# Performance work log

Measured on AMD Instinct MI355X. Metric: run time of the kernel, lower is better.

The kernel has to match this reference:

```python
import jax, jax.numpy as jnp
import numpy as np

EPS = 1e-5

def _bn(x, g, b):
    m = x.mean(axis=0)
    v = x.var(axis=0)  # biased, matches torch BN training normalization
    return g * (x - m) * jax.lax.rsqrt(v + EPS) + b

def _mlp(x, W1, b1, g1, be1, W2, b2, g2, be2):
    h = jax.nn.relu(_bn(x @ W1 + b1, g1, be1))
    return jax.nn.relu(_bn(h @ W2 + b2, g2, be2))

def setup_inputs() -> dict:
    key = jax.random.key(0)
    ks = jax.random.split(key, 12)
    n, e, d, de = 100000, 1600000, 128, 16
    def lin(k, fan_in, fan_out):
        bound = 1.0 / np.sqrt(fan_in)
        k1, k2 = jax.random.split(k)
        W = jax.random.uniform(k1, (fan_in, fan_out), jnp.float32, -bound, bound)
        b = jax.random.uniform(k2, (fan_out,), jnp.float32, -bound, bound)
        return W, b
    msg_W1, msg_b1 = lin(ks[0], 2 * d + de, d)
    msg_W2, msg_b2 = lin(ks[1], d, d)
    upd_W1, upd_b1 = lin(ks[2], 3 * d, d)
    upd_W2, upd_b2 = lin(ks[3], d, d)
    return {
        "h": jax.random.normal(ks[4], (n, d), jnp.float32),
        "edge_index": jax.random.randint(ks[5], (2, e), 0, n, jnp.int64),
        "edge_attr": jax.random.normal(ks[6], (e, de), jnp.float32),
        "msg_W1": msg_W1, "msg_b1": msg_b1,
        "msg_g1": jnp.ones((d,)), "msg_be1": jnp.zeros((d,)),
        "msg_W2": msg_W2, "msg_b2": msg_b2,
        "msg_g2": jnp.ones((d,)), "msg_be2": jnp.zeros((d,)),
        "upd_W1": upd_W1, "upd_b1": upd_b1,
        "upd_g1": jnp.ones((d,)), "upd_be1": jnp.zeros((d,)),
        "upd_W2": upd_W2, "upd_b2": upd_b2,
        "upd_g2": jnp.ones((d,)), "upd_be2": jnp.zeros((d,)),
    }

def reference(h, edge_index, edge_attr,
              msg_W1, msg_b1, msg_g1, msg_be1, msg_W2, msg_b2, msg_g2, msg_be2,
              upd_W1, upd_b1, upd_g1, upd_be1, upd_W2, upd_b2, upd_g2, upd_be2):
    alpha = 0.5
    n = h.shape[0]
    src = edge_index[0]
    dst = edge_index[1]
    h_i = h[src]  # (e, d)
    h_j = h[dst]  # (e, d)
    msg_args = (msg_W1, msg_b1, msg_g1, msg_be1, msg_W2, msg_b2, msg_g2, msg_be2)
    m_st = _mlp(jnp.concatenate([h_i, h_j, edge_attr], axis=-1), *msg_args)
    m_ts = _mlp(jnp.concatenate([h_j, h_i, edge_attr], axis=-1), *msg_args)
    # NOTE: original code scatters both directions by source nodes (faithful)
    a_st = jax.ops.segment_sum(m_st, src, num_segments=n)
    a_ts = jax.ops.segment_sum(m_ts, src, num_segments=n)
    upd_in = jnp.concatenate([h, alpha * a_st, (1.0 - alpha) * a_ts], axis=-1)
    return _mlp(upd_in, upd_W1, upd_b1, upd_g1, upd_be1, upd_W2, upd_b2, upd_g2, upd_be2)
```

## Files before the change

kernel.cpp:

```cpp
#include <hip/hip_runtime.h>

#define EPS_BN 1e-5f

typedef __bf16 bf16x8 __attribute__((ext_vector_type(8)));
typedef float f32x4 __attribute__((ext_vector_type(4)));
typedef unsigned short us8 __attribute__((ext_vector_type(8)));
typedef unsigned int u32x4 __attribute__((ext_vector_type(4)));

__device__ __forceinline__ unsigned short f2bf(float x) {
  unsigned u = __builtin_bit_cast(unsigned, x);
  unsigned r = (u + 0x7fffu + ((u >> 16) & 1u)) >> 16;
  return (unsigned short)r;
}
__device__ __forceinline__ unsigned pack2bf(float a, float b) {
  return (unsigned)f2bf(a) | ((unsigned)f2bf(b) << 16);
}
__device__ __forceinline__ unsigned long long pack4bf(float a, float b, float c, float d) {
  return (unsigned long long)pack2bf(a, b) | ((unsigned long long)pack2bf(c, d) << 32);
}
__device__ __forceinline__ float ubf(unsigned short u) {
  return __builtin_bit_cast(float, (unsigned)u << 16);
}

template <bool ABF16>
__global__ __launch_bounds__(256) void node_mfma(
    const void* A0, const void* A1, const void* A2,
    const float* __restrict__ W, float s0, float s1, float s2,
    float* __restrict__ C, int n, int dostats,
    float* __restrict__ sum_out, float* __restrict__ ssq_out, int nk) {
  __shared__ unsigned short WT[128][136];
  int tid = threadIdx.x;
  int lid = tid & 63, w = tid >> 6, lr = lid & 15, lq = lid >> 4;
  long rbase = (long)blockIdx.x * 64 + 16 * w;

  const void* As[3] = {A0, A1, A2};
  float ss[3] = {s0, s1, s2};
  f32x4 acc[8];
  #pragma unroll
  for (int nf = 0; nf < 8; ++nf) acc[nf] = f32x4{0.f, 0.f, 0.f, 0.f};

  long r = rbase + lr;
  bool rv = (r < n);
  long rl = rv ? r : 0;

  for (int c = 0; c < nk; ++c) {
    if (c) __syncthreads();
    const float* Wc = W + (long)c * 16384;
    float sc = ss[c];
    for (int i = tid; i < 16384; i += 256) {
      int k = i >> 7, cc = i & 127;
      WT[cc][k] = f2bf(Wc[i] * sc);
    }
    __syncthreads();

    bf16x8 af[4];
    if (ABF16) {
      const us8* Ar = (const us8*)((const unsigned short*)As[c] + rl * 128);
      #pragma unroll
      for (int ks = 0; ks < 4; ++ks) {
        us8 v = Ar[ks * 4 + lq];
        if (!rv) v = us8{0, 0, 0, 0, 0, 0, 0, 0};
        af[ks] = __builtin_bit_cast(bf16x8, v);
      }
    } else {
      const float* Ar = (const float*)As[c] + rl * 128;
      #pragma unroll
      for (int ks = 0; ks < 4; ++ks) {
        int e0 = 32 * ks + 8 * lq;
        float4 x = *(const float4*)(Ar + e0);
        float4 y = *(const float4*)(Ar + e0 + 4);
        u32x4 t;
        t[0] = pack2bf(x.x, x.y); t[1] = pack2bf(x.z, x.w);
        t[2] = pack2bf(y.x, y.y); t[3] = pack2bf(y.z, y.w);
        if (!rv) { t[0] = 0; t[1] = 0; t[2] = 0; t[3] = 0; }
        af[ks] = __builtin_bit_cast(bf16x8, t);
      }
    }
    #pragma unroll
    for (int nf = 0; nf < 8; ++nf) {
      const char* bp = (const char*)&WT[16 * nf + lr][0];
      #pragma unroll
      for (int ks = 0; ks < 4; ++ks) {
        bf16x8 bf = *(const bf16x8*)(bp + ks * 64 + lq * 16);
        acc[nf] = __builtin_amdgcn_mfma_f32_16x16x32_bf16(af[ks], bf, acc[nf], 0, 0, 0);
      }
    }
  }

  float lsum[8], lssq[8];
  #pragma unroll
  for (int nf = 0; nf < 8; ++nf) { lsum[nf] = 0.f; lssq[nf] = 0.f; }
  #pragma unroll
  for (int nf = 0; nf < 8; ++nf) {
    #pragma unroll
    for (int i = 0; i < 4; ++i) {
      long nd = rbase + 4 * lq + i;
      if (nd < n) {
        float v = acc[nf][i];
        C[nd * 128 + 16 * nf + lr] = v;
        lsum[nf] += v; lssq[nf] += v * v;
      }
    }
  }
  if (dostats) {
    #pragma unroll
    for (int nf = 0; nf < 8; ++nf) {
      float v0 = lsum[nf]; v0 += __shfl_xor(v0, 16); v0 += __shfl_xor(v0, 32);
      float v1 = lssq[nf]; v1 += __shfl_xor(v1, 16); v1 += __shfl_xor(v1, 32);
      if (lq == 0) {
        atomicAdd(&sum_out[16 * nf + lr], v0);
        atomicAdd(&ssq_out[16 * nf + lr], v1);
      }
    }
  }
}

__global__ __launch_bounds__(256) void msg_stats1(
    const float* __restrict__ P, const float* __restrict__ Q,
    const float* __restrict__ EA, const float* __restrict__ W1e,
    const int* __restrict__ SRC, const int* __restrict__ DST, long E,
    float* __restrict__ stats) {
  __shared__ float Wel[16][128];
  __shared__ float red[32][16];
  int tid = threadIdx.x;
  for (int i = tid; i < 16 * 128; i += 256) ((float*)Wel)[i] = W1e[i];
  for (int i = tid; i < 512; i += 256) ((float*)red)[i] = 0.f;
  __syncthreads();
  int c4 = tid & 31, grp = tid >> 5;
  const float4* P4 = (const float4*)P;
  const float4* Q4 = (const float4*)Q;
  float4 s_st = {0,0,0,0}, q_st = {0,0,0,0}, s_ts = {0,0,0,0}, q_ts = {0,0,0,0};
  long stride = (long)gridDim.x * 8;
  for (long e = (long)blockIdx.x * 8 + grp; e < E; e += stride) {
    int s = SRC[e], t = DST[e];
    float4 Ps = P4[(long)s * 32 + c4];
    float4 Qt = Q4[(long)t * 32 + c4];
    float4 Pt = P4[(long)t * 32 + c4];
    float4 Qs = Q4[(long)s * 32 + c4];
    float rx = 0.f, ry = 0.f, rz = 0.f, rw = 0.f;
    const float* eap = EA + e * 16;
    #pragma unroll
    for (int k = 0; k < 16; ++k) {
      float f = eap[k];
      const float4 w4 = *(const float4*)&Wel[k][c4 * 4];
      rx = fmaf(f, w4.x, rx); ry = fmaf(f, w4.y, ry);
      rz = fmaf(f, w4.z, rz); rw = fmaf(f, w4.w, rw);
    }
    float zx = Ps.x + Qt.x + rx, zy = Ps.y + Qt.y + ry, zz = Ps.z + Qt.z + rz, zw = Ps.w + Qt.w + rw;
    s_st.x += zx; s_st.y += zy; s_st.z += zz; s_st.w += zw;
    q_st.x += zx * zx; q_st.y += zy * zy; q_st.z += zz * zz; q_st.w += zw * zw;
    float ux = Pt.x + Qs.x + rx, uy = Pt.y + Qs.y + ry, uz = Pt.z + Qs.z + rz, uw = Pt.w + Qs.w + rw;
    s_ts.x += ux; s_ts.y += uy; s_ts.z += uz; s_ts.w += uw;
    q_ts.x += ux * ux; q_ts.y += uy * uy; q_ts.z += uz * uz; q_ts.w += uw * uw;
  }
  atomicAdd(&red[c4][0], s_st.x);  atomicAdd(&red[c4][1], s_st.y);
  atomicAdd(&red[c4][2], s_st.z);  atomicAdd(&red[c4][3], s_st.w);
  atomicAdd(&red[c4][4], q_st.x);  atomicAdd(&red[c4][5], q_st.y);
  atomicAdd(&red[c4][6], q_st.z);  atomicAdd(&red[c4][7], q_st.w);
  atomicAdd(&red[c4][8], s_ts.x);  atomicAdd(&red[c4][9], s_ts.y);
  atomicAdd(&red[c4][10], s_ts.z); atomicAdd(&red[c4][11], s_ts.w);
  atomicAdd(&red[c4][12], q_ts.x); atomicAdd(&red[c4][13], q_ts.y);
  atomicAdd(&red[c4][14], q_ts.z); atomicAdd(&red[c4][15], q_ts.w);
  __syncthreads();
  #pragma unroll
  for (int rep = 0; rep < 2; ++rep) {
    int j = rep * 256 + tid;
    int cc = j >> 4, k = j & 15, group = k >> 2, comp = k & 3;
    atomicAdd(&stats[group * 128 + cc * 4 + comp], red[cc][k]);
  }
}

__global__ __launch_bounds__(256) void prescale_pq(
    const float* __restrict__ X, const float* __restrict__ sca,
    const float* __restrict__ scb,
    unsigned* __restrict__ outA, unsigned* __restrict__ outB, long nrows) {
  long gid = (long)blockIdx.x * 256 + threadIdx.x;
  int c2 = (int)(gid & 63);
  float a0 = sca[2 * c2], a1 = sca[2 * c2 + 1];
  float b0 = scb[2 * c2], b1 = scb[2 * c2 + 1];
  const float2* X2 = (const float2*)X;
  long rstride = ((long)gridDim.x * 256) >> 6;
  for (long row = gid >> 6; row < nrows; row += rstride) {
    float2 x = X2[row * 64 + c2];
    outA[row * 64 + c2] = pack2bf(x.x * a0, x.y * a1);
    outB[row * 64 + c2] = pack2bf(x.x * b0, x.y * b1);
  }
}

__global__ __launch_bounds__(256) void prescale_relu(
    const float* __restrict__ X, const float* __restrict__ scsh,
    unsigned* __restrict__ out, long nrows) {
  long gid = (long)blockIdx.x * 256 + threadIdx.x;
  int c2 = (int)(gid & 63);
  float s0 = scsh[2 * c2], s1 = scsh[2 * c2 + 1];
  float h0 = scsh[128 + 2 * c2], h1 = scsh[128 + 2 * c2 + 1];
  const float2* X2 = (const float2*)X;
  long rstride = ((long)gridDim.x * 256) >> 6;
  for (long row = gid >> 6; row < nrows; row += rstride) {
    float2 x = X2[row * 64 + c2];
    out[row * 64 + c2] = pack2bf(fmaxf(fmaf(x.x, s0, h0), 0.f),
                                 fmaxf(fmaf(x.y, s1, h1), 0.f));
  }
}

__global__ __launch_bounds__(256) void rmat_scaled(
    const float* __restrict__ EA, const float* __restrict__ W1e,
    const float* __restrict__ sc1,
    unsigned* __restrict__ Rst, unsigned* __restrict__ Rts, long E) {
  long gid = (long)blockIdx.x * 256 + threadIdx.x;
  int c2 = (int)(gid & 63);
  int ch = 2 * c2;
  float wa[16], wb[16];
  #pragma unroll
  for (int k = 0; k < 16; ++k) { wa[k] = W1e[k * 128 + ch]; wb[k] = W1e[k * 128 + ch + 1]; }
  float sa_st = sc1[ch],       sb_st = sc1[ch + 1];
  float ha_st = sc1[128 + ch], hb_st = sc1[128 + ch + 1];
  float sa_ts = sc1[256 + ch], sb_ts = sc1[256 + ch + 1];
  float ha_ts = sc1[384 + ch], hb_ts = sc1[384 + ch + 1];
  long estride = ((long)gridDim.x * 256) >> 6;
  for (long e = gid >> 6; e < E; e += estride) {
    const float* eap = EA + e * 16;
    float ra = 0.f, rb = 0.f;
    #pragma unroll
    for (int k = 0; k < 16; ++k) { ra = fmaf(eap[k], wa[k], ra); rb = fmaf(eap[k], wb[k], rb); }
    Rst[e * 64 + c2] = pack2bf(fmaf(ra, sa_st, ha_st), fmaf(rb, sb_st, hb_st));
    Rts[e * 64 + c2] = pack2bf(fmaf(ra, sa_ts, ha_ts), fmaf(rb, sb_ts, hb_ts));
  }
}

template <bool SCATTER>
__global__ __launch_bounds__(256) void msg2(
    const unsigned short* __restrict__ Pst, const unsigned short* __restrict__ Qst,
    const unsigned short* __restrict__ Pts, const unsigned short* __restrict__ Qts,
    const unsigned short* __restrict__ Rst, const unsigned short* __restrict__ Rts,
    const float* __restrict__ W2,
    const int* __restrict__ SRC, const int* __restrict__ DST, long E,
    const float* __restrict__ sc2, float* __restrict__ stats2,
    float* __restrict__ a_st, float* __restrict__ a_ts) {
  __shared__ unsigned short W2T[128][136];
  int tid = threadIdx.x;
  for (int i = tid; i < 16384; i += 256) {
    int k = i >> 7, c = i & 127;
    W2T[c][k] = f2bf(W2[i]);
  }
  __syncthreads();
  int lid = tid & 63, w = tid >> 6, lr = lid & 15, lq = lid >> 4;

  float s2st[8], h2st[8], s2ts[8], h2ts[8];
  float sum_st[8], ssq_st[8], sum_ts[8], ssq_ts[8];
  if constexpr (SCATTER) {
    #pragma unroll
    for (int nf = 0; nf < 8; ++nf) {
      int ch = 16 * nf + lr;
      s2st[nf] = sc2[ch];       h2st[nf] = sc2[128 + ch];
      s2ts[nf] = sc2[256 + ch]; h2ts[nf] = sc2[384 + ch];
    }
  } else {
    #pragma unroll
    for (int nf = 0; nf < 8; ++nf) {
      sum_st[nf] = 0.f; ssq_st[nf] = 0.f; sum_ts[nf] = 0.f; ssq_ts[nf] = 0.f;
    }
  }

  for (long wbase = (long)blockIdx.x * 64 + 16 * w; wbase < E;
       wbase += (long)gridDim.x * 64) {
    long e = wbase + lr;
    bool ev = (e < E);
    long el = ev ? e : (E - 1);
    int s = SRC[el], t = DST[el];
    const us8* PstR = (const us8*)(Pst + (long)s * 128);
    const us8* QstR = (const us8*)(Qst + (long)t * 128);
    const us8* PtsR = (const us8*)(Pts + (long)t * 128);
    const us8* QtsR = (const us8*)(Qts + (long)s * 128);
    const us8* RstR = (const us8*)(Rst + el * 128);
    const us8* RtsR = (const us8*)(Rts + el * 128);

    bf16x8 afst[4], afts[4];
    #pragma unroll
    for (int ks = 0; ks < 4; ++ks) {
      int ci = ks * 4 + lq;
      us8 p1 = PstR[ci], q1 = QstR[ci], r1 = RstR[ci];
      us8 p2 = PtsR[ci], q2 = QtsR[ci], r2 = RtsR[ci];
      u32x4 t1, t2;
      #pragma unroll
      for (int jj = 0; jj < 4; ++jj) {
        float a0 = fmaxf(ubf(p1[2 * jj]) + ubf(q1[2 * jj]) + ubf(r1[2 * jj]), 0.f);
        float a1 = fmaxf(ubf(p1[2 * jj + 1]) + ubf(q1[2 * jj + 1]) + ubf(r1[2 * jj + 1]), 0.f);
        float b0 = fmaxf(ubf(p2[2 * jj]) + ubf(q2[2 * jj]) + ubf(r2[2 * jj]), 0.f);
        float b1 = fmaxf(ubf(p2[2 * jj + 1]) + ubf(q2[2 * jj + 1]) + ubf(r2[2 * jj + 1]), 0.f);
        t1[jj] = pack2bf(a0, a1);
        t2[jj] = pack2bf(b0, b1);
      }
      if (!ev) { t1[0]=0; t1[1]=0; t1[2]=0; t1[3]=0; t2[0]=0; t2[1]=0; t2[2]=0; t2[3]=0; }
      afst[ks] = __builtin_bit_cast(bf16x8, t1);
      afts[ks] = __builtin_bit_cast(bf16x8, t2);
    }

    int srow[4];
    if constexpr (SCATTER) {
      #pragma unroll
      for (int i = 0; i < 4; ++i) {
        long er = wbase + 4 * lq + i;
        srow[i] = (er < E) ? SRC[er] : -1;
      }
    }

    #pragma unroll
    for (int nf = 0; nf < 8; ++nf) {
      f32x4 acc_st = {0.f, 0.f, 0.f, 0.f};
      f32x4 acc_ts = {0.f, 0.f, 0.f, 0.f};
      const char* bp = (const char*)&W2T[16 * nf + lr][0];
      #pragma unroll
      for (int ks = 0; ks < 4; ++ks) {
        bf16x8 bf = *(const bf16x8*)(bp + ks * 64 + lq * 16);
        acc_st = __builtin_amdgcn_mfma_f32_16x16x32_bf16(afst[ks], bf, acc_st, 0, 0, 0);
        acc_ts = __builtin_amdgcn_mfma_f32_16x16x32_bf16(afts[ks], bf, acc_ts, 0, 0, 0);
      }
      if constexpr (SCATTER) {
        int ch = 16 * nf + lr;
        #pragma unroll
        for (int i = 0; i < 4; ++i) {
          if (srow[i] >= 0) {
            float m1 = fmaxf(fmaf(acc_st[i], s2st[nf], h2st[nf]), 0.f);
            float m2 = fmaxf(fmaf(acc_ts[i], s2ts[nf], h2ts[nf]), 0.f);
            if (m1 > 0.f) atomicAdd(&a_st[(long)srow[i] * 128 + ch], m1);
            if (m2 > 0.f) atomicAdd(&a_ts[(long)srow[i] * 128 + ch], m2);
          }
        }
      } else {
        #pragma unroll
        for (int i = 0; i < 4; ++i) {
          sum_st[nf] += acc_st[i]; ssq_st[nf] += acc_st[i] * acc_st[i];
          sum_ts[nf] += acc_ts[i]; ssq_ts[nf] += acc_ts[i] * acc_ts[i];
        }
      }
    }
  }

  if constexpr (!SCATTER) {
    #pragma unroll
    for (int nf = 0; nf < 8; ++nf) {
      float v0 = sum_st[nf]; v0 += __shfl_xor(v0, 16); v0 += __shfl_xor(v0, 32);
      float v1 = ssq_st[nf]; v1 += __shfl_xor(v1, 16); v1 += __shfl_xor(v1, 32);
      float v2 = sum_ts[nf]; v2 += __shfl_xor(v2, 16); v2 += __shfl_xor(v2, 32);
      float v3 = ssq_ts[nf]; v3 += __shfl_xor(v3, 16); v3 += __shfl_xor(v3, 32);
      if (lq == 0) {
        int ch = 16 * nf + lr;
        atomicAdd(&stats2[ch], v0);
        atomicAdd(&stats2[128 + ch], v1);
        atomicAdd(&stats2[256 + ch], v2);
        atomicAdd(&stats2[384 + ch], v3);
      }
    }
  }
}

template <bool SCATTER>
__global__ __launch_bounds__(256) void msg_mfma_kernel(
    const float* __restrict__ P, const float* __restrict__ Q,
    const float* __restrict__ EA, const float* __restrict__ W1e,
    const float* __restrict__ W2,
    const int* __restrict__ SRC, const int* __restrict__ DST, long E,
    const float* __restrict__ sc1, const float* __restrict__ sc2,
    float* __restrict__ stats2,
    float* __restrict__ a_st, float* __restrict__ a_ts) {
  __shared__ unsigned short W2T[128][136];
  __shared__ unsigned short Ast[64][136];
  __shared__ unsigned short Ats[64][136];
  __shared__ float Wel[16][128];
  __shared__ int sArr[64];

  int tid = threadIdx.x;
  int c4 = tid & 31;
  int slot = tid >> 5;
  int lid = tid & 63;
  int w = tid >> 6;
  int lr = lid & 15;
  int lq = lid >> 4;

  for (int i = tid; i < 16 * 128; i += 256) ((float*)Wel)[i] = W1e[i];
  #pragma unroll
  for (int i = 0; i < 64; ++i) {
    int idx = i * 256 + tid;
    int k = idx >> 7, n = idx & 127;
    W2T[n][k] = f2bf(W2[idx]);
  }

  const float4* sc1v = (const float4*)sc1;
  float4 scst = sc1v[c4], shst = sc1v[32 + c4];
  float4 scts = sc1v[64 + c4], shts = sc1v[96 + c4];

  float s2st[8], h2st[8], s2ts[8], h2ts[8];
  if constexpr (SCATTER) {
    #pragma unroll
    for (int nf = 0; nf < 8; ++nf) {
      int ch = 16 * nf + lr;
      s2st[nf] = sc2[ch];       h2st[nf] = sc2[128 + ch];
      s2ts[nf] = sc2[256 + ch]; h2ts[nf] = sc2[384 + ch];
    }
  }
  float ssum_st[8], sssq_st[8], ssum_ts[8], sssq_ts[8];
  if constexpr (!SCATTER) {
    #pragma unroll
    for (int nf = 0; nf < 8; ++nf) {
      ssum_st[nf] = 0.f; sssq_st[nf] = 0.f; ssum_ts[nf] = 0.f; sssq_ts[nf] = 0.f;
    }
  }

  const float4* P4 = (const float4*)P;
  const float4* Q4 = (const float4*)Q;

  for (long tb = (long)blockIdx.x * 64; tb < E; tb += (long)gridDim.x * 64) {
    int nE = (int)(E - tb < 64 ? E - tb : 64);
    __syncthreads();
    #pragma unroll 2
    for (int rep = 0; rep < 8; ++rep) {
      int er = rep * 8 + slot;
      if (er < nE) {
        long e = tb + er;
        int s = SRC[e], t = DST[e];
        if (SCATTER && c4 == 0) sArr[er] = s;
        float4 Ps = P4[(long)s * 32 + c4];
        float4 Qt = Q4[(long)t * 32 + c4];
        float4 Pt = P4[(long)t * 32 + c4];
        float4 Qs = Q4[(long)s * 32 + c4];
        float rx = 0.f, ry = 0.f, rz = 0.f, rw = 0.f;
        const float* eap = EA + e * 16;
        #pragma unroll
        for (int k = 0; k < 16; ++k) {
          float f = eap[k];
          const float4 w4 = *(const float4*)&Wel[k][c4 * 4];
          rx = fmaf(f, w4.x, rx); ry = fmaf(f, w4.y, ry);
          rz = fmaf(f, w4.z, rz); rw = fmaf(f, w4.w, rw);
        }
        float ax = fmaxf(fmaf(Ps.x + Qt.x + rx, scst.x, shst.x), 0.f);
        float ay = fmaxf(fmaf(Ps.y + Qt.y + ry, scst.y, shst.y), 0.f);
        float az = fmaxf(fmaf(Ps.z + Qt.z + rz, scst.z, shst.z), 0.f);
        float aw = fmaxf(fmaf(Ps.w + Qt.w + rw, scst.w, shst.w), 0.f);
        *(unsigned long long*)&Ast[er][c4 * 4] = pack4bf(ax, ay, az, aw);
        float bx = fmaxf(fmaf(Pt.x + Qs.x + rx, scts.x, shts.x), 0.f);
        float by = fmaxf(fmaf(Pt.y + Qs.y + ry, scts.y, shts.y), 0.f);
        float bz = fmaxf(fmaf(Pt.z + Qs.z + rz, scts.z, shts.z), 0.f);
        float bw = fmaxf(fmaf(Pt.w + Qs.w + rw, scts.w, shts.w), 0.f);
        *(unsigned long long*)&Ats[er][c4 * 4] = pack4bf(bx, by, bz, bw);
      } else {
        *(unsigned long long*)&Ast[er][c4 * 4] = 0ull;
        *(unsigned long long*)&Ats[er][c4 * 4] = 0ull;
      }
    }
    __syncthreads();

    int arow = 16 * w + lr;
    const char* astp = (const char*)&Ast[arow][0];
    const char* atsp = (const char*)&Ats[arow][0];
    int acolb = lq * 16;
    bf16x8 afst[4], afts[4];
    #pragma unroll
    for (int ks = 0; ks < 4; ++ks) {
      afst[ks] = *(const bf16x8*)(astp + ks * 64 + acolb);
      afts[ks] = *(const bf16x8*)(atsp + ks * 64 + acolb);
    }
    int srow[4];
    if constexpr (SCATTER) {
      #pragma unroll
      for (int i = 0; i < 4; ++i) {
        int row = 16 * w + 4 * lq + i;
        srow[i] = (row < nE) ? sArr[row] : -1;
      }
    }
    #pragma unroll
    for (int nf = 0; nf < 8; ++nf) {
      f32x4 acc_st = {0.f, 0.f, 0.f, 0.f};
      f32x4 acc_ts = {0.f, 0.f, 0.f, 0.f};
      const char* bp = (const char*)&W2T[16 * nf + lr][0];
      #pragma unroll
      for (int ks = 0; ks < 4; ++ks) {
        bf16x8 bf = *(const bf16x8*)(bp + ks * 64 + acolb);
        acc_st = __builtin_amdgcn_mfma_f32_16x16x32_bf16(afst[ks], bf, acc_st, 0, 0, 0);
        acc_ts = __builtin_amdgcn_mfma_f32_16x16x32_bf16(afts[ks], bf, acc_ts, 0, 0, 0);
      }
      if constexpr (SCATTER) {
        int ch = 16 * nf + lr;
        #pragma unroll
        for (int i = 0; i < 4; ++i) {
          if (srow[i] >= 0) {
            float m1 = fmaxf(fmaf(acc_st[i], s2st[nf], h2st[nf]), 0.f);
            float m2 = fmaxf(fmaf(acc_ts[i], s2ts[nf], h2ts[nf]), 0.f);
            if (m1 > 0.f) atomicAdd(&a_st[(long)srow[i] * 128 + ch], m1);
            if (m2 > 0.f) atomicAdd(&a_ts[(long)srow[i] * 128 + ch], m2);
          }
        }
      } else {
        #pragma unroll
        for (int i = 0; i < 4; ++i) {
          ssum_st[nf] += acc_st[i]; sssq_st[nf] += acc_st[i] * acc_st[i];
          ssum_ts[nf] += acc_ts[i]; sssq_ts[nf] += acc_ts[i] * acc_ts[i];
        }
      }
    }
  }

  if constexpr (!SCATTER) {
    #pragma unroll
    for (int nf = 0; nf < 8; ++nf) {
      float v0 = ssum_st[nf]; v0 += __shfl_xor(v0, 16); v0 += __shfl_xor(v0, 32);
      float v1 = sssq_st[nf]; v1 += __shfl_xor(v1, 16); v1 += __shfl_xor(v1, 32);
      float v2 = ssum_ts[nf]; v2 += __shfl_xor(v2, 16); v2 += __shfl_xor(v2, 32);
      float v3 = sssq_ts[nf]; v3 += __shfl_xor(v3, 16); v3 += __shfl_xor(v3, 32);
      if (lq == 0) {
        int ch = 16 * nf + lr;
        atomicAdd(&stats2[ch], v0);
        atomicAdd(&stats2[128 + ch], v1);
        atomicAdd(&stats2[256 + ch], v2);
        atomicAdd(&stats2[384 + ch], v3);
      }
    }
  }
}

__global__ void bn_finalize(const float* __restrict__ sum, const float* __restrict__ ssq,
                            float invN, const float* __restrict__ g,
                            const float* __restrict__ be,
                            float* __restrict__ sc, float* __restrict__ sh) {
  int j = threadIdx.x;
  float m = sum[j] * invN;
  float v = ssq[j] * invN - m * m;
  float s = g[j] * rsqrtf(v + EPS_BN);
  sc[j] = s;
  sh[j] = be[j] - m * s;
}

__global__ __launch_bounds__(256) void bn_relu_out(
    const float* __restrict__ U2, const float* __restrict__ scsh,
    float* __restrict__ out, long total) {
  long i = (long)blockIdx.x * blockDim.x + threadIdx.x;
  long stride = (long)gridDim.x * blockDim.x;
  for (; i < total; i += stride) {
    int j = (int)(i & 127);
    out[i] = fmaxf(fmaf(U2[i], scsh[j], scsh[128 + j]), 0.f);
  }
}

extern "C" void kernel_launch(void* const* d_in, const int* in_sizes, int n_in,
                              void* d_out, int out_size, void* d_ws, size_t ws_size,
                              hipStream_t stream) {
  const float* h    = (const float*)d_in[0];
  const int*   ei   = (const int*)d_in[1];
  const float* ea   = (const float*)d_in[2];
  const float* mW1  = (const float*)d_in[3];
  const float* mg1  = (const float*)d_in[5];
  const float* mbe1 = (const float*)d_in[6];
  const float* mW2  = (const float*)d_in[7];
  const float* mg2  = (const float*)d_in[9];
  const float* mbe2 = (const float*)d_in[10];
  const float* uW1  = (const float*)d_in[11];
  const float* ug1  = (const float*)d_in[13];
  const float* ube1 = (const float*)d_in[14];
  const float* uW2  = (const float*)d_in[15];
  const float* ug2  = (const float*)d_in[17];
  const float* ube2 = (const float*)d_in[18];

  int n = in_sizes[0] / 128;
  long E = (long)(in_sizes[1] / 2);
  const int* SRC = ei;
  const int* DST = ei + E;
  const float* W1e = mW1 + 256 * 128;

  size_t nf = (size_t)n * 128;
  float* P    = (float*)d_ws;
  float* Q    = P + nf;
  float* a_st = Q + nf;
  float* a_ts = a_st + nf;
  float* st   = a_ts + nf;

  char* fastbase = (char*)(st + 3072);
  unsigned short* Pst = (unsigned short*)fastbase;
  unsigned short* Qst = Pst + nf;
  unsigned short* Pts = Qst + nf;
  unsigned short* Qts = Pts + nf;
  unsigned short* Rst = Qts + nf;
  unsigned short* Rts = Rst + (size_t)E * 128;
  size_t need = (size_t)((char*)(Rts + (size_t)E * 128) - (char*)d_ws);
  bool fast = (ws_size >= need);

  float invE = 1.0f / (float)E;
  float invN = 1.0f / (float)n;
  int nblk = (n + 63) / 64;

  hipMemsetAsync((char*)d_ws + 2 * nf * sizeof(float), 0,
                 (2 * nf + 3072) * sizeof(float), stream);

  node_mfma<false><<<nblk, 256, 0, stream>>>(h, nullptr, nullptr, mW1, 1.f, 0.f, 0.f,
                                             P, n, 0, nullptr, nullptr, 1);
  node_mfma<false><<<nblk, 256, 0, stream>>>(h, nullptr, nullptr, mW1 + 16384, 1.f, 0.f, 0.f,
                                             Q, n, 0, nullptr, nullptr, 1);

  msg_stats1<<<2048, 256, 0, stream>>>(P, Q, ea, W1e, SRC, DST, E, st);
  bn_finalize<<<1, 128, 0, stream>>>(st + 0,   st + 128, invE, mg1, mbe1, st + 1536, st + 1664);
  bn_finalize<<<1, 128, 0, stream>>>(st + 256, st + 384, invE, mg1, mbe1, st + 1792, st + 1920);

  if (fast) {
    prescale_pq<<<2048, 256, 0, stream>>>(P, st + 1536, st + 1792,
                                          (unsigned*)Pst, (unsigned*)Pts, n);
    prescale_pq<<<2048, 256, 0, stream>>>(Q, st + 1536, st + 1792,
                                          (unsigned*)Qst, (unsigned*)Qts, n);
    rmat_scaled<<<2048, 256, 0, stream>>>(ea, W1e, st + 1536,
                                          (unsigned*)Rst, (unsigned*)Rts, E);
    msg2<false><<<2048, 256, 0, stream>>>(Pst, Qst, Pts, Qts, Rst, Rts, mW2,
                                          SRC, DST, E, nullptr, st + 512, nullptr, nullptr);
    bn_finalize<<<1, 128, 0, stream>>>(st + 512, st + 640, invE, mg2, mbe2, st + 2048, st + 2176);
    bn_finalize<<<1, 128, 0, stream>>>(st + 768, st + 896, invE, mg2, mbe2, st + 2304, st + 2432);
    msg2<true><<<2048, 256, 0, stream>>>(Pst, Qst, Pts, Qts, Rst, Rts, mW2,
                                         SRC, DST, E, st + 2048, nullptr, a_st, a_ts);
  } else {
    msg_mfma_kernel<false><<<1024, 256, 0, stream>>>(
        P, Q, ea, W1e, mW2, SRC, DST, E, st + 1536, nullptr, st + 512, nullptr, nullptr);
    bn_finalize<<<1, 128, 0, stream>>>(st + 512, st + 640, invE, mg2, mbe2, st + 2048, st + 2176);
    bn_finalize<<<1, 128, 0, stream>>>(st + 768, st + 896, invE, mg2, mbe2, st + 2304, st + 2432);
    msg_mfma_kernel<true><<<1024, 256, 0, stream>>>(
        P, Q, ea, W1e, mW2, SRC, DST, E, st + 1536, st + 2048, nullptr, a_st, a_ts);
  }

  node_mfma<false><<<nblk, 256, 0, stream>>>(h, a_st, a_ts, uW1, 1.f, 0.5f, 0.5f,
                                             P, n, 1, st + 1024, st + 1152, 3);
  bn_finalize<<<1, 128, 0, stream>>>(st + 1024, st + 1152, invN, ug1, ube1, st + 2560, st + 2688);

  unsigned short* u1p = (unsigned short*)a_st;
  prescale_relu<<<2048, 256, 0, stream>>>(P, st + 2560, (unsigned*)u1p, n);
  node_mfma<true><<<nblk, 256, 0, stream>>>(u1p, nullptr, nullptr, uW2, 1.f, 0.f, 0.f,
                                            Q, n, 1, st + 1280, st + 1408, 1);
  bn_finalize<<<1, 128, 0, stream>>>(st + 1280, st + 1408, invN, ug2, ube2, st + 2816, st + 2944);

  bn_relu_out<<<2048, 256, 0, stream>>>(Q, st + 2816, (float*)d_out, (long)n * 128);
}
```

Baseline: 2.902 ms.

## Chunk per-edge R tables and reuse workspace to enable fast path in small workspace

Restructures workspace so the fast bf16 table path no longer needs full per-edge Rst/Rts buffers. Edges are processed in chunks sized to the remaining workspace, and each chunk's R matrix is recomputed before each msg2 pass. The BN shift is folded into the P tables rather than R, and node buffers are aliased to free space. It also lays weights out in LDS in MFMA fragment order for conflict-free contiguous loads. The cost is recomputing R twice and launching more kernels.

```diff
diff --git a/kernel.cpp b/kernel.cpp
--- a/kernel.cpp
+++ b/kernel.cpp
@@ -20,6 +20,11 @@
 }
 __device__ __forceinline__ float ubf(unsigned short u) {
   return __builtin_bit_cast(float, (unsigned)u << 16);
+}
+
+__device__ __forceinline__ int fragidx(int k, int c) {
+  int nf = c >> 4, lr = c & 15, ks = k >> 5, lq = (k >> 3) & 3, j = k & 7;
+  return ((((nf << 2) + ks) << 6) | (lq << 4) | lr) * 8 + j;
 }
 
 template <bool ABF16>
@@ -28,7 +33,7 @@
     const float* __restrict__ W, float s0, float s1, float s2,
     float* __restrict__ C, int n, int dostats,
     float* __restrict__ sum_out, float* __restrict__ ssq_out, int nk) {
-  __shared__ unsigned short WT[128][136];
+  __shared__ unsigned short WT[16384];
   int tid = threadIdx.x;
   int lid = tid & 63, w = tid >> 6, lr = lid & 15, lq = lid >> 4;
   long rbase = (long)blockIdx.x * 64 + 16 * w;
@@ -42,14 +47,14 @@
   long r = rbase + lr;
   bool rv = (r < n);
   long rl = rv ? r : 0;
+  const us8* WF8 = (const us8*)WT;
 
   for (int c = 0; c < nk; ++c) {
     if (c) __syncthreads();
     const float* Wc = W + (long)c * 16384;
     float sc = ss[c];
     for (int i = tid; i < 16384; i += 256) {
-      int k = i >> 7, cc = i & 127;
-      WT[cc][k] = f2bf(Wc[i] * sc);
+      WT[fragidx(i >> 7, i & 127)] = f2bf(Wc[i] * sc);
     }
     __syncthreads();
 
@@ -78,10 +83,9 @@
     }
     #pragma unroll
     for (int nf = 0; nf < 8; ++nf) {
-      const char* bp = (const char*)&WT[16 * nf + lr][0];
       #pragma unroll
       for (int ks = 0; ks < 4; ++ks) {
-        bf16x8 bf = *(const bf16x8*)(bp + ks * 64 + lq * 16);
+        bf16x8 bf = __builtin_bit_cast(bf16x8, WF8[(nf * 4 + ks) * 64 + lid]);
         acc[nf] = __builtin_amdgcn_mfma_f32_16x16x32_bf16(af[ks], bf, acc[nf], 0, 0, 0);
       }
     }
@@ -170,20 +174,27 @@
   }
 }
 
-__global__ __launch_bounds__(256) void prescale_pq(
-    const float* __restrict__ X, const float* __restrict__ sca,
-    const float* __restrict__ scb,
-    unsigned* __restrict__ outA, unsigned* __restrict__ outB, long nrows) {
+__global__ __launch_bounds__(256) void prescale_tables(
+    const float* __restrict__ X,
+    const float* __restrict__ sa, const float* __restrict__ ha,
+    const float* __restrict__ sb, const float* __restrict__ hb,
+    unsigned* __restrict__ outA, unsigned* __restrict__ outB,
+    long nrows, int with_sh) {
   long gid = (long)blockIdx.x * 256 + threadIdx.x;
   int c2 = (int)(gid & 63);
-  float a0 = sca[2 * c2], a1 = sca[2 * c2 + 1];
-  float b0 = scb[2 * c2], b1 = scb[2 * c2 + 1];
+  float a0 = sa[2 * c2], a1 = sa[2 * c2 + 1];
+  float b0 = sb[2 * c2], b1 = sb[2 * c2 + 1];
+  float ha0 = 0.f, ha1 = 0.f, hb0 = 0.f, hb1 = 0.f;
+  if (with_sh) {
+    ha0 = ha[2 * c2]; ha1 = ha[2 * c2 + 1];
+    hb0 = hb[2 * c2]; hb1 = hb[2 * c2 + 1];
+  }
   const float2* X2 = (const float2*)X;
   long rstride = ((long)gridDim.x * 256) >> 6;
   for (long row = gid >> 6; row < nrows; row += rstride) {
     float2 x = X2[row * 64 + c2];
-    outA[row * 64 + c2] = pack2bf(x.x * a0, x.y * a1);
-    outB[row * 64 + c2] = pack2bf(x.x * b0, x.y * b1);
+    outA[row * 64 + c2] = pack2bf(fmaf(x.x, a0, ha0), fmaf(x.y, a1, ha1));
+    outB[row * 64 + c2] = pack2bf(fmaf(x.x, b0, hb0), fmaf(x.y, b1, hb1));
   }
 }
 
@@ -203,28 +214,26 @@
   }
 }
 
-__global__ __launch_bounds__(256) void rmat_scaled(
+__global__ __launch_bounds__(256) void rmat_chunk(
     const float* __restrict__ EA, const float* __restrict__ W1e,
-    const float* __restrict__ sc1,
-    unsigned* __restrict__ Rst, unsigned* __restrict__ Rts, long E) {
+    const float* __restrict__ sc_st, const float* __restrict__ sc_ts,
+    unsigned* __restrict__ Rst, unsigned* __restrict__ Rts, long csz) {
   long gid = (long)blockIdx.x * 256 + threadIdx.x;
   int c2 = (int)(gid & 63);
   int ch = 2 * c2;
   float wa[16], wb[16];
   #pragma unroll
   for (int k = 0; k < 16; ++k) { wa[k] = W1e[k * 128 + ch]; wb[k] = W1e[k * 128 + ch + 1]; }
-  float sa_st = sc1[ch],       sb_st = sc1[ch + 1];
-  float ha_st = sc1[128 + ch], hb_st = sc1[128 + ch + 1];
-  float sa_ts = sc1[256 + ch], sb_ts = sc1[256 + ch + 1];
-  float ha_ts = sc1[384 + ch], hb_ts = sc1[384 + ch + 1];
+  float sa_st = sc_st[ch], sb_st = sc_st[ch + 1];
+  float sa_ts = sc_ts[ch], sb_ts = sc_ts[ch + 1];
   long estride = ((long)gridDim.x * 256) >> 6;
-  for (long e = gid >> 6; e < E; e += estride) {
+  for (long e = gid >> 6; e < csz; e += estride) {
     const float* eap = EA + e * 16;
     float ra = 0.f, rb = 0.f;
     #pragma unroll
     for (int k = 0; k < 16; ++k) { ra = fmaf(eap[k], wa[k], ra); rb = fmaf(eap[k], wb[k], rb); }
-    Rst[e * 64 + c2] = pack2bf(fmaf(ra, sa_st, ha_st), fmaf(rb, sb_st, hb_st));
-    Rts[e * 64 + c2] = pack2bf(fmaf(ra, sa_ts, ha_ts), fmaf(rb, sb_ts, hb_ts));
+    Rst[e * 64 + c2] = pack2bf(ra * sa_st, rb * sb_st);
+    Rts[e * 64 + c2] = pack2bf(ra * sa_ts, rb * sb_ts);
   }
 }
 
@@ -234,16 +243,17 @@
     const unsigned short* __restrict__ Pts, const unsigned short* __restrict__ Qts,
     const unsigned short* __restrict__ Rst, const unsigned short* __restrict__ Rts,
     const float* __restrict__ W2,
-    const int* __restrict__ SRC, const int* __restrict__ DST, long E,
+    const int* __restrict__ SRC, const int* __restrict__ DST,
+    long cbase, long csz,
     const float* __restrict__ sc2, float* __restrict__ stats2,
     float* __restrict__ a_st, float* __restrict__ a_ts) {
-  __shared__ unsigned short W2T[128][136];
+  __shared__ unsigned short W2F[16384];
   int tid = threadIdx.x;
   for (int i = tid; i < 16384; i += 256) {
-    int k = i >> 7, c = i & 127;
-    W2T[c][k] = f2bf(W2[i]);
+    W2F[fragidx(i >> 7, i & 127)] = f2bf(W2[i]);
   }
   __syncthreads();
+  const us8* W2F8 = (const us8*)W2F;
   int lid = tid & 63, w = tid >> 6, lr = lid & 15, lq = lid >> 4;
 
   float s2st[8], h2st[8], s2ts[8], h2ts[8];
@@ -262,18 +272,19 @@
     }
   }
 
-  for (long wbase = (long)blockIdx.x * 64 + 16 * w; wbase < E;
-       wbase += (long)gridDim.x * 64) {
-    long e = wbase + lr;
-    bool ev = (e < E);
-    long el = ev ? e : (E - 1);
-    int s = SRC[el], t = DST[el];
+  for (long wb = (long)blockIdx.x * 64 + 16 * w; wb < csz;
+       wb += (long)gridDim.x * 64) {
+    long le = wb + lr;
+    bool ev = (le < csz);
+    long lel = ev ? le : (csz - 1);
+    long e = cbase + lel;
+    int s = SRC[e], t = DST[e];
     const us8* PstR = (const us8*)(Pst + (long)s * 128);
     const us8* QstR = (const us8*)(Qst + (long)t * 128);
     const us8* PtsR = (const us8*)(Pts + (long)t * 128);
     const us8* QtsR = (const us8*)(Qts + (long)s * 128);
-    const us8* RstR = (const us8*)(Rst + el * 128);
-    const us8* RtsR = (const us8*)(Rts + el * 128);
+    const us8* RstR = (const us8*)(Rst + lel * 128);
+    const us8* RtsR = (const us8*)(Rts + lel * 128);
 
     bf16x8 afst[4], afts[4];
     #pragma unroll
@@ -281,27 +292,27 @@
       int ci = ks * 4 + lq;
       us8 p1 = PstR[ci], q1 = QstR[ci], r1 = RstR[ci];
       us8 p2 = PtsR[ci], q2 = QtsR[ci], r2 = RtsR[ci];
-      u32x4 t1, t2;
-      #pragma unroll
-      for (int jj = 0; jj < 4; ++jj) {
-        float a0 = fmaxf(ubf(p1[2 * jj]) + ubf(q1[2 * jj]) + ubf(r1[2 * jj]), 0.f);
-        float a1 = fmaxf(ubf(p1[2 * jj + 1]) + ubf(q1[2 * jj + 1]) + ubf(r1[2 * jj + 1]), 0.f);
-        float b0 = fmaxf(ubf(p2[2 * jj]) + ubf(q2[2 * jj]) + ubf(r2[2 * jj]), 0.f);
-        float b1 = fmaxf(ubf(p2[2 * jj + 1]) + ubf(q2[2 * jj + 1]) + ubf(r2[2 * jj + 1]), 0.f);
-        t1[jj] = pack2bf(a0, a1);
-        t2[jj] = pack2bf(b0, b1);
-      }
-      if (!ev) { t1[0]=0; t1[1]=0; t1[2]=0; t1[3]=0; t2[0]=0; t2[1]=0; t2[2]=0; t2[3]=0; }
-      afst[ks] = __builtin_bit_cast(bf16x8, t1);
-      afts[ks] = __builtin_bit_cast(bf16x8, t2);
+      bf16x8 o1, o2;
+      #pragma unroll
+      for (int j = 0; j < 8; ++j) {
+        float a = fmaxf(ubf(p1[j]) + ubf(q1[j]) + ubf(r1[j]), 0.f);
+        float b = fmaxf(ubf(p2[j]) + ubf(q2[j]) + ubf(r2[j]), 0.f);
+        o1[j] = (__bf16)a;
+        o2[j] = (__bf16)b;
+      }
+      if (!ev) {
+        o1 = __builtin_bit_cast(bf16x8, us8{0,0,0,0,0,0,0,0});
+        o2 = __builtin_bit_cast(bf16x8, us8{0,0,0,0,0,0,0,0});
+      }
+      afst[ks] = o1; afts[ks] = o2;
     }
 
     int srow[4];
     if constexpr (SCATTER) {
       #pragma unroll
       for (int i = 0; i < 4; ++i) {
-        long er = wbase + 4 * lq + i;
-        srow[i] = (er < E) ? SRC[er] : -1;
+        long ler = wb + 4 * lq + i;
+        srow[i] = (ler < csz) ? SRC[cbase + ler] : -1;
       }
     }
 
@@ -309,10 +320,9 @@
     for (int nf = 0; nf < 8; ++nf) {
       f32x4 acc_st = {0.f, 0.f, 0.f, 0.f};
       f32x4 acc_ts = {0.f, 0.f, 0.f, 0.f};
-      const char* bp = (const char*)&W2T[16 * nf + lr][0];
       #pragma unroll
       for (int ks = 0; ks < 4; ++ks) {
-        bf16x8 bf = *(const bf16x8*)(bp + ks * 64 + lq * 16);
+        bf16x8 bf = __builtin_bit_cast(bf16x8, W2F8[(nf * 4 + ks) * 64 + lid]);
         acc_st = __builtin_amdgcn_mfma_f32_16x16x32_bf16(afst[ks], bf, acc_st, 0, 0, 0);
         acc_ts = __builtin_amdgcn_mfma_f32_16x16x32_bf16(afts[ks], bf, acc_ts, 0, 0, 0);
       }
@@ -567,69 +577,115 @@
   const float* W1e = mW1 + 256 * 128;
 
   size_t nf = (size_t)n * 128;
-  float* P    = (float*)d_ws;
-  float* Q    = P + nf;
-  float* a_st = Q + nf;
-  float* a_ts = a_st + nf;
-  float* st   = a_ts + nf;
-
-  char* fastbase = (char*)(st + 3072);
-  unsigned short* Pst = (unsigned short*)fastbase;
-  unsigned short* Qst = Pst + nf;
-  unsigned short* Pts = Qst + nf;
-  unsigned short* Qts = Pts + nf;
-  unsigned short* Rst = Qts + nf;
-  unsigned short* Rts = Rst + (size_t)E * 128;
-  size_t need = (size_t)((char*)(Rts + (size_t)E * 128) - (char*)d_ws);
-  bool fast = (ws_size >= need);
+  float* bufA = (float*)d_ws;
+  float* bufB = bufA + nf;
+  float* st   = bufB + nf;
+  unsigned short* tab = (unsigned short*)(st + 3072);
+  unsigned short* Pst = tab;
+  unsigned short* Qst = tab + nf;
+  unsigned short* Pts = tab + 2 * nf;
+  unsigned short* Qts = tab + 3 * nf;
+  unsigned short* Rst = tab + 4 * nf;
+
+  size_t used = (size_t)((char*)Rst - (char*)d_ws);
+  long rcap = (ws_size > used) ? (long)((ws_size - used) / 512) : 0;
+  long RCHUNK = rcap & ~63L;
+  if (RCHUNK > E) RCHUNK = E;
+  bool fast = (RCHUNK >= 65536);
+  unsigned short* Rts = Rst + (size_t)RCHUNK * 128;
 
   float invE = 1.0f / (float)E;
   float invN = 1.0f / (float)n;
   int nblk = (n + 63) / 64;
 
-  hipMemsetAsync((char*)d_ws + 2 * nf * sizeof(float), 0,
-                 (2 * nf + 3072) * sizeof(float), stream);
-
-  node_mfma<false><<<nblk, 256, 0, stream>>>(h, nullptr, nullptr, mW1, 1.f, 0.f, 0.f,
-                                             P, n, 0, nullptr, nullptr, 1);
-  node_mfma<false><<<nblk, 256, 0, stream>>>(h, nullptr, nullptr, mW1 + 16384, 1.f, 0.f, 0.f,
-                                             Q, n, 0, nullptr, nullptr, 1);
-
-  msg_stats1<<<2048, 256, 0, stream>>>(P, Q, ea, W1e, SRC, DST, E, st);
-  bn_finalize<<<1, 128, 0, stream>>>(st + 0,   st + 128, invE, mg1, mbe1, st + 1536, st + 1664);
-  bn_finalize<<<1, 128, 0, stream>>>(st + 256, st + 384, invE, mg1, mbe1, st + 1792, st + 1920);
-
   if (fast) {
-    prescale_pq<<<2048, 256, 0, stream>>>(P, st + 1536, st + 1792,
-                                          (unsigned*)Pst, (unsigned*)Pts, n);
-    prescale_pq<<<2048, 256, 0, stream>>>(Q, st + 1536, st + 1792,
-                                          (unsigned*)Qst, (unsigned*)Qts, n);
-    rmat_scaled<<<2048, 256, 0, stream>>>(ea, W1e, st + 1536,
-                                          (unsigned*)Rst, (unsigned*)Rts, E);
-    msg2<false><<<2048, 256, 0, stream>>>(Pst, Qst, Pts, Qts, Rst, Rts, mW2,
-                                          SRC, DST, E, nullptr, st + 512, nullptr, nullptr);
+    hipMemsetAsync(st, 0, 3072 * sizeof(float), stream);
+
+    node_mfma<false><<<nblk, 256, 0, stream>>>(h, nullptr, nullptr, mW1, 1.f, 0.f, 0.f,
+                                               bufA, n, 0, nullptr, nullptr, 1);
+    node_mfma<false><<<nblk, 256, 0, stream>>>(h, nullptr, nullptr, mW1 + 16384, 1.f, 0.f, 0.f,
+                                               bufB, n, 0, nullptr, nullptr, 1);
+
+    msg_stats1<<<2048, 256, 0, stream>>>(bufA, bufB, ea, W1e, SRC, DST, E, st);
+    bn_finalize<<<1, 128, 0, stream>>>(st + 0,   st + 128, invE, mg1, mbe1, st + 1536, st + 1664);
+    bn_finalize<<<1, 128, 0, stream>>>(st + 256, st + 384, invE, mg1, mbe1, st + 1792, st + 1920);
+
+    prescale_tables<<<2048, 256, 0, stream>>>(bufA, st + 1536, st + 1664, st + 1792, st + 1920,
+                                              (unsigned*)Pst, (unsigned*)Pts, n, 1);
+    prescale_tables<<<2048, 256, 0, stream>>>(bufB, st + 1536, nullptr, st + 1792, nullptr,
+                                              (unsigned*)Qst, (unsigned*)Qts, n, 0);
+
+    hipMemsetAsync(bufA, 0, 2 * nf * sizeof(float), stream);
+
+    for (long cb = 0; cb < E; cb += RCHUNK) {
+      long csz = (E - cb < RCHUNK) ? (E - cb) : RCHUNK;
+      rmat_chunk<<<4096, 256, 0, stream>>>(ea + cb * 16, W1e, st + 1536, st + 1792,
+                                           (unsigned*)Rst, (unsigned*)Rts, csz);
+      int g = (int)((csz + 63) / 64);
+      msg2<false><<<g, 256, 0, stream>>>(Pst, Qst, Pts, Qts, Rst, Rts, mW2,
+                                         SRC, DST, cb, csz, nullptr, st + 512,
+                                         nullptr, nullptr);
+    }
     bn_finalize<<<1, 128, 0, stream>>>(st + 512, st + 640, invE, mg2, mbe2, st + 2048, st + 2176);
     bn_finalize<<<1, 128, 0, stream>>>(st + 768, st + 896, invE, mg2, mbe2, st + 2304, st + 2432);
-    msg2<true><<<2048, 256, 0, stream>>>(Pst, Qst, Pts, Qts, Rst, Rts, mW2,
-                                         SRC, DST, E, st + 2048, nullptr, a_st, a_ts);
+
+    for (long cb = 0; cb < E; cb += RCHUNK) {
+      long csz = (E - cb < RCHUNK) ? (E - cb) : RCHUNK;
+      rmat_chunk<<<4096, 256, 0, stream>>>(ea + cb * 16, W1e, st + 1536, st + 1792,
+                                           (unsigned*)Rst, (unsigned*)Rts, csz);
+      int g = (int)((csz + 63) / 64);
+      msg2<true><<<g, 256, 0, stream>>>(Pst, Qst, Pts, Qts, Rst, Rts, mW2,
+                                        SRC, DST, cb, csz, st + 2048, nullptr,
+                                        bufA, bufB);
+    }
+
+    float* u1 = (float*)tab;
+    unsigned short* u1p = (unsigned short*)(u1 + nf);
+    node_mfma<false><<<nblk, 256, 0, stream>>>(h, bufA, bufB, uW1, 1.f, 0.5f, 0.5f,
+                                               u1, n, 1, st + 1024, st + 1152, 3);
+    bn_finalize<<<1, 128, 0, stream>>>(st + 1024, st + 1152, invN, ug1, ube1, st + 2560, st + 2688);
+
+    prescale_relu<<<2048, 256, 0, stream>>>(u1, st + 2560, (unsigned*)u1p, n);
+    node_mfma<true><<<nblk, 256, 0, stream>>>(u1p, nullptr, nullptr, uW2, 1.f, 0.f, 0.f,
+                                              bufA, n, 1, st + 1280, st + 1408, 1);
+    bn_finalize<<<1, 128, 0, stream>>>(st + 1280, st + 1408, invN, ug2, ube2, st + 2816, st + 2944);
+
+    bn_relu_out<<<2048, 256, 0, stream>>>(bufA, st + 2816, (float*)d_out, (long)n * 128);
   } else {
+    float* P    = bufA;
+    float* Q    = bufB;
+    float* a_st = (float*)tab;
+    float* a_ts = a_st + nf;
+
+    hipMemsetAsync(st, 0, 3072 * sizeof(float), stream);
+    hipMemsetAsync(a_st, 0, 2 * nf * sizeof(float), stream);
+
+    node_mfma<false><<<nblk, 256, 0, stream>>>(h, nullptr, nullptr, mW1, 1.f, 0.f, 0.f,
+                                               P, n, 0, nullptr, nullptr, 1);
+    node_mfma<false><<<nblk, 256, 0, stream>>>(h, nullptr, nullptr, mW1 + 16384, 1.f, 0.f, 0.f,
+                                               Q, n, 0, nullptr, nullptr, 1);
+
+    msg_stats1<<<2048, 256, 0, stream>>>(P, Q, ea, W1e, SRC, DST, E, st);
+    bn_finalize<<<1, 128, 0, stream>>>(st + 0,   st + 128, invE, mg1, mbe1, st + 1536, st + 1664);
+    bn_finalize<<<1, 128, 0, stream>>>(st + 256, st + 384, invE, mg1, mbe1, st + 1792, st + 1920);
+
     msg_mfma_kernel<false><<<1024, 256, 0, stream>>>(
         P, Q, ea, W1e, mW2, SRC, DST, E, st + 1536, nullptr, st + 512, nullptr, nullptr);
     bn_finalize<<<1, 128, 0, stream>>>(st + 512, st + 640, invE, mg2, mbe2, st + 2048, st + 2176);
     bn_finalize<<<1, 128, 0, stream>>>(st + 768, st + 896, invE, mg2, mbe2, st + 2304, st + 2432);
     msg_mfma_kernel<true><<<1024, 256, 0, stream>>>(
         P, Q, ea, W1e, mW2, SRC, DST, E, st + 1536, st + 2048, nullptr, a_st, a_ts);
-  }
-
-  node_mfma<false><<<nblk, 256, 0, stream>>>(h, a_st, a_ts, uW1, 1.f, 0.5f, 0.5f,
-                                             P, n, 1, st + 1024, st + 1152, 3);
-  bn_finalize<<<1, 128, 0, stream>>>(st + 1024, st + 1152, invN, ug1, ube1, st + 2560, st + 2688);
-
-  unsigned short* u1p = (unsigned short*)a_st;
-  prescale_relu<<<2048, 256, 0, stream>>>(P, st + 2560, (unsigned*)u1p, n);
-  node_mfma<true><<<nblk, 256, 0, stream>>>(u1p, nullptr, nullptr, uW2, 1.f, 0.f, 0.f,
-                                            Q, n, 1, st + 1280, st + 1408, 1);
-  bn_finalize<<<1, 128, 0, stream>>>(st + 1280, st + 1408, invN, ug2, ube2, st + 2816, st + 2944);
-
-  bn_relu_out<<<2048, 256, 0, stream>>>(Q, st + 2816, (float*)d_out, (long)n * 128);
-}
+
+    node_mfma<false><<<nblk, 256, 0, stream>>>(h, a_st, a_ts, uW1, 1.f, 0.5f, 0.5f,
+                                               P, n, 1, st + 1024, st + 1152, 3);
+    bn_finalize<<<1, 128, 0, stream>>>(st + 1024, st + 1152, invN, ug1, ube1, st + 2560, st + 2688);
+
+    unsigned short* u1p = (unsigned short*)a_st;
+    prescale_relu<<<2048, 256, 0, stream>>>(P, st + 2560, (unsigned*)u1p, n);
+    node_mfma<true><<<nblk, 256, 0, stream>>>(u1p, nullptr, nullptr, uW2, 1.f, 0.f, 0.f,
+                                              Q, n, 1, st + 1280, st + 1408, 1);
+    bn_finalize<<<1, 128, 0, stream>>>(st + 1280, st + 1408, invN, ug2, ube2, st + 2816, st + 2944);
+
+    bn_relu_out<<<2048, 256, 0, stream>>>(Q, st + 2816, (float*)d_out, (long)n * 128);
+  }
+}
```

New measurement: 6.144 ms. 112% more time.
